# Kernel optimization log

Hardware: AMD Instinct MI355X
Metric: run time of the kernel (lower is better)

Reference implementation:

```python
import jax, jax.numpy as jnp
import numpy as np


def setup_inputs() -> dict:
    key = jax.random.key(0)
    ks = jax.random.split(key, 6)
    B, T, U = 4, 160, 80
    De, Dd = 640, 640
    inner, vocab = 640, 1024
    return {
        "enc_state": jax.random.normal(ks[0], (B, T, De), jnp.float32),
        "dec_state": jax.random.normal(ks[1], (B, U, Dd), jnp.float32),
        "W1": jax.random.normal(ks[2], (De + Dd, inner), jnp.float32) * (1.0 / np.sqrt(De + Dd)),
        "b1": jax.random.normal(ks[3], (inner,), jnp.float32) * 0.02,
        "W2": jax.random.normal(ks[4], (inner, vocab), jnp.float32) * (1.0 / np.sqrt(inner)),
        "b2": jax.random.normal(ks[5], (vocab,), jnp.float32) * 0.02,
    }


def reference(enc_state, dec_state, W1, b1, W2, b2):
    # Faithful to: cat([enc tiled over U, dec tiled over T], -1) @ W1 + b1,
    # algebraically split so the [B,T,U,2D] concat is never materialized:
    # cat(e, d) @ W1 == e @ W1[:De] + d @ W1[De:]
    De = enc_state.shape[-1]
    W1_enc, W1_dec = W1[:De], W1[De:]
    enc_proj = jnp.einsum("btd,dh->bth", enc_state, W1_enc)   # [B,T,H]
    dec_proj = jnp.einsum("bud,dh->buh", dec_state, W1_dec)   # [B,U,H]
    # broadcast add over the (T,U) lattice -> [B,T,U,H]
    hidden = jnp.tanh(enc_proj[:, :, None, :] + dec_proj[:, None, :, :] + b1)
    logits = jnp.einsum("btuh,hv->btuv", hidden, W2) + b2     # [B,T,U,V]
    return logits
```

## Files before the change

### kernel.cpp

```cpp
#include <hip/hip_runtime.h>
#include <hip/hip_bf16.h>
#include <cstdint>

#define D_    640
#define V_    1024
#define M_    51200

typedef __bf16 bf16x8 __attribute__((ext_vector_type(8)));
typedef float floatx4 __attribute__((ext_vector_type(4)));

__device__ __forceinline__ void g2l16(const void* g, void* l) {
    __builtin_amdgcn_global_load_lds((const __attribute__((address_space(1))) void*)g,
                                     (__attribute__((address_space(3))) void*)l,
                                     16, 0, 0);
}

__device__ __forceinline__ float fast_tanh(float x) {
    float e = __builtin_amdgcn_exp2f(x * 2.8853900817779268f);
    return 1.0f - 2.0f * __builtin_amdgcn_rcpf(e + 1.0f);
}

__global__ __launch_bounds__(256) void proj_kernel(
    const float* __restrict__ enc, const float* __restrict__ dec,
    const float* __restrict__ W1, const float* __restrict__ b1,
    float* __restrict__ encp, float* __restrict__ decp) {
    __shared__ float As[64][36];
    __shared__ float Ws[32][68];

    const int rt = blockIdx.y;
    const int ct = blockIdx.x;
    const bool is_enc = (rt < 10);
    const float* Asrc; const float* Wsrc; float* Cdst;
    if (is_enc) { Asrc = enc + (size_t)rt * 64 * D_;        Wsrc = W1;           Cdst = encp + (size_t)rt * 64 * D_; }
    else        { Asrc = dec + (size_t)(rt - 10) * 64 * D_; Wsrc = W1 + D_ * D_; Cdst = decp + (size_t)(rt - 10) * 64 * D_; }

    const int tid = threadIdx.x;
    const int ar = tid >> 2,  ac = (tid & 3) * 8;
    const int wr2 = tid >> 3, wc2 = (tid & 7) * 8;
    const int tr = tid >> 4,  tc = tid & 15;

    float acc[4][4] = {};
    for (int k0 = 0; k0 < D_; k0 += 32) {
        __syncthreads();
        *(floatx4*)&As[ar][ac]       = *(const floatx4*)&Asrc[(size_t)ar * D_ + k0 + ac];
        *(floatx4*)&As[ar][ac + 4]   = *(const floatx4*)&Asrc[(size_t)ar * D_ + k0 + ac + 4];
        *(floatx4*)&Ws[wr2][wc2]     = *(const floatx4*)&Wsrc[(size_t)(k0 + wr2) * D_ + ct * 64 + wc2];
        *(floatx4*)&Ws[wr2][wc2 + 4] = *(const floatx4*)&Wsrc[(size_t)(k0 + wr2) * D_ + ct * 64 + wc2 + 4];
        __syncthreads();
#pragma unroll
        for (int kk = 0; kk < 32; kk++) {
            floatx4 w = *(const floatx4*)&Ws[kk][tc * 4];
            float a0 = As[tr * 4 + 0][kk], a1 = As[tr * 4 + 1][kk];
            float a2 = As[tr * 4 + 2][kk], a3 = As[tr * 4 + 3][kk];
#pragma unroll
            for (int j = 0; j < 4; j++) {
                acc[0][j] += a0 * w[j]; acc[1][j] += a1 * w[j];
                acc[2][j] += a2 * w[j]; acc[3][j] += a3 * w[j];
            }
        }
    }
    floatx4 bv = {0.f, 0.f, 0.f, 0.f};
    if (is_enc) bv = *(const floatx4*)&b1[ct * 64 + tc * 4];
#pragma unroll
    for (int i = 0; i < 4; i++) {
        floatx4 v = { acc[i][0] + bv[0], acc[i][1] + bv[1],
                      acc[i][2] + bv[2], acc[i][3] + bv[3] };
        *(floatx4*)&Cdst[(size_t)(tr * 4 + i) * D_ + ct * 64 + tc * 4] = v;
    }
}

__global__ __launch_bounds__(256) void w2t_kernel(
    const float* __restrict__ W2, __bf16* __restrict__ W2t) {
    __shared__ __bf16 tile[32][33];
    const int vt = blockIdx.x;
    const int kt = blockIdx.y;
    const int tx = threadIdx.x & 31, ty = threadIdx.x >> 5;
#pragma unroll
    for (int i = 0; i < 4; i++)
        tile[ty + i * 8][tx] = (__bf16)W2[(size_t)(kt * 32 + ty + i * 8) * V_ + vt * 32 + tx];
    __syncthreads();
#pragma unroll
    for (int i = 0; i < 4; i++)
        W2t[(size_t)(vt * 32 + ty + i * 8) * D_ + kt * 32 + tx] = tile[tx][ty + i * 8];
}

__global__ __launch_bounds__(256, 2) void joint_kernel(
    const float* __restrict__ encp, const float* __restrict__ decp,
    const __bf16* __restrict__ W2t, const float* __restrict__ b2,
    float* __restrict__ C) {
    __shared__ __align__(128) char lds[81920];

    const int bid = blockIdx.x;
    const int swz = (bid & 7) * 200 + (bid >> 3);
    const int mt = swz >> 2, nt = swz & 3;
    const int m0 = mt * 128, n0 = nt * 256;

    const int tid = threadIdx.x;
    const int w = tid >> 6, l = tid & 63;
    const int lr = l & 15, lk = l >> 4;

    char* ldsp = (char*)lds;

    const char* Wb = (const char*)W2t
        + (size_t)(n0 + (tid >> 3)) * 1280
        + (unsigned)((((tid & 7) ^ ((tid >> 3) & 7)) * 16));
    const unsigned bdst = 16384u + (unsigned)tid * 16u;

    const int pr = tid >> 1;
    const int kh = (tid & 1) * 32;
    const int R  = m0 + pr;
    const int bt = R / 80;
    const int uu = R - bt * 80;
    const int drw = (bt / 160) * 80 + uu;
    const float* ep = encp + (size_t)bt * D_ + kh;
    const float* dp = decp + (size_t)drw * D_ + kh;
    const unsigned prb = (unsigned)(pr * 128);
    const unsigned ps0 = (unsigned)((tid & 1) * 4);
    const unsigned px  = (unsigned)(pr & 7);

    floatx4 acc[8][4] = {};

#define STAGE_B(BUF, T) do { \
    const char* _s = Wb + (size_t)(T) * 128; \
    char* _d = ldsp + bdst + (BUF) * 32768; \
    g2l16(_s,           _d); \
    g2l16(_s +  40960,  _d +  4096); \
    g2l16(_s +  81920,  _d +  8192); \
    g2l16(_s + 122880,  _d + 12288); \
    g2l16(_s + 163840,  _d + 16384); \
    g2l16(_s + 204800,  _d + 20480); \
    g2l16(_s + 245760,  _d + 24576); \
    g2l16(_s + 286720,  _d + 28672); \
  } while (0)

#define PRODUCE_A(T) do { \
    _Pragma("unroll") for (int sub = 0; sub < 2; ++sub) { \
      const float* _e = ep + (T) * 64 + sub * 16; \
      const float* _d = dp + (T) * 64 + sub * 16; \
      floatx4 ev[4], dv[4]; \
      _Pragma("unroll") for (int q = 0; q < 4; ++q) { \
        ev[q] = *(const floatx4*)(_e + q * 4); \
        dv[q] = *(const floatx4*)(_d + q * 4); \
      } \
      bf16x8 h0, h1; \
      _Pragma("unroll") for (int q = 0; q < 4; ++q) { \
        _Pragma("unroll") for (int i2 = 0; i2 < 4; ++i2) { \
          float t_ = fast_tanh(ev[q][i2] + dv[q][i2]); \
          if (q < 2) h0[q * 4 + i2] = (__bf16)t_; else h1[(q - 2) * 4 + i2] = (__bf16)t_; \
        } } \
      *(bf16x8*)(ldsp + prb + (((ps0 + sub * 2)     ^ px) * 16)) = h0; \
      *(bf16x8*)(ldsp + prb + (((ps0 + sub * 2 + 1) ^ px) * 16)) = h1; \
    } } while (0)

#define FRAGS_MFMA(BUF) do { \
    _Pragma("unroll") \
    for (int s = 0; s < 2; ++s) { \
        const unsigned sx = (unsigned)((((s * 4 + lk) ^ (lr & 7)) * 16)); \
        bf16x8 af[8], bfr[4]; \
        _Pragma("unroll") for (int i = 0; i < 8; ++i) \
            af[i] = *(const bf16x8*)(ldsp + (i * 16 + lr) * 128 + sx); \
        _Pragma("unroll") for (int j = 0; j < 4; ++j) \
            bfr[j] = *(const bf16x8*)(ldsp + 16384 + (BUF) * 32768 + (w * 64 + j * 16 + lr) * 128 + sx); \
        _Pragma("unroll") for (int i = 0; i < 8; ++i) \
            _Pragma("unroll") for (int j = 0; j < 4; ++j) \
                acc[i][j] = __builtin_amdgcn_mfma_f32_16x16x32_bf16(af[i], bfr[j], acc[i][j], 0, 0, 0); \
    } } while (0)

    STAGE_B(0, 0);
    PRODUCE_A(0);
    __syncthreads();

#pragma unroll 1
    for (int t = 0; t < 9; ++t) {
        const int buf = t & 1, nb = buf ^ 1;
        FRAGS_MFMA(buf);
        __syncthreads();
        STAGE_B(nb, t + 1);
        PRODUCE_A(t + 1);
        __syncthreads();
    }
    FRAGS_MFMA(1);

#pragma unroll
    for (int j = 0; j < 4; ++j) {
        const int col = n0 + w * 64 + j * 16 + lr;
        const float bj = b2[col];
#pragma unroll
        for (int i = 0; i < 8; ++i) {
            const int row = m0 + i * 16 + lk * 4;
            float* Cp = C + (size_t)row * V_ + col;
#pragma unroll
            for (int rg = 0; rg < 4; ++rg)
                Cp[(size_t)rg * V_] = acc[i][j][rg] + bj;
        }
    }
#undef STAGE_B
#undef PRODUCE_A
#undef FRAGS_MFMA
}

extern "C" void kernel_launch(void* const* d_in, const int* in_sizes, int n_in,
                              void* d_out, int out_size, void* d_ws, size_t ws_size,
                              hipStream_t stream) {
    const float* enc = (const float*)d_in[0];
    const float* dec = (const float*)d_in[1];
    const float* W1  = (const float*)d_in[2];
    const float* b1  = (const float*)d_in[3];
    const float* W2  = (const float*)d_in[4];
    const float* b2  = (const float*)d_in[5];
    float* out = (float*)d_out;

    char* ws = (char*)d_ws;
    float*  encp = (float*)ws;
    float*  decp = (float*)(ws + 1638400);
    __bf16* W2t  = (__bf16*)(ws + 1638400 + 819200);

    proj_kernel<<<dim3(10, 15), 256, 0, stream>>>(enc, dec, W1, b1, encp, decp);
    w2t_kernel<<<dim3(32, 20), 256, 0, stream>>>(W2, W2t);
    joint_kernel<<<1600, 256, 0, stream>>>(encp, decp, W2t, b2, out);
}
```

Measured before the change: 369.3 us.

## Load W2 fragments directly to registers, halve M tile, transpose MFMA for vector stores

The joint kernel stops staging W2t through LDS with global_load_lds. Each wave now loads its B fragments straight from global memory into double-buffered registers. The M tile is halved to 64 rows, so the grid doubles to 3200 blocks and LDS shrinks to 16 KB, which should raise occupancy. MFMA operands are swapped so each lane holds four consecutive columns, which allows float4 output stores and a float4 bias load. The trade-off is redundant W2 global reads per block, since each 256-column B tile now serves only 64 rows, plus reliance on L2 for B reuse and hand-placed barriers.

```diff
diff --git a/kernel.cpp b/kernel.cpp
--- a/kernel.cpp
+++ b/kernel.cpp
@@ -8,12 +8,6 @@
 
 typedef __bf16 bf16x8 __attribute__((ext_vector_type(8)));
 typedef float floatx4 __attribute__((ext_vector_type(4)));
-
-__device__ __forceinline__ void g2l16(const void* g, void* l) {
-    __builtin_amdgcn_global_load_lds((const __attribute__((address_space(1))) void*)g,
-                                     (__attribute__((address_space(3))) void*)l,
-                                     16, 0, 0);
-}
 
 __device__ __forceinline__ float fast_tanh(float x) {
     float e = __builtin_amdgcn_exp2f(x * 2.8853900817779268f);
@@ -88,12 +82,12 @@
     const float* __restrict__ encp, const float* __restrict__ decp,
     const __bf16* __restrict__ W2t, const float* __restrict__ b2,
     float* __restrict__ C) {
-    __shared__ __align__(128) char lds[81920];
+    __shared__ __align__(128) char lds[16384];
 
     const int bid = blockIdx.x;
-    const int swz = (bid & 7) * 200 + (bid >> 3);
+    const int swz = (bid & 7) * 400 + (bid >> 3);
     const int mt = swz >> 2, nt = swz & 3;
-    const int m0 = mt * 128, n0 = nt * 256;
+    const int m0 = mt * 64, n0 = nt * 256;
 
     const int tid = threadIdx.x;
     const int w = tid >> 6, l = tid & 63;
@@ -102,101 +96,97 @@
     char* ldsp = (char*)lds;
 
     const char* Wb = (const char*)W2t
-        + (size_t)(n0 + (tid >> 3)) * 1280
-        + (unsigned)((((tid & 7) ^ ((tid >> 3) & 7)) * 16));
-    const unsigned bdst = 16384u + (unsigned)tid * 16u;
-
-    const int pr = tid >> 1;
-    const int kh = (tid & 1) * 32;
+        + (size_t)(n0 + w * 64 + lr) * 1280 + (unsigned)(lk * 16);
+
+    const int pr = tid >> 2;
+    const int kq = tid & 3;
     const int R  = m0 + pr;
     const int bt = R / 80;
     const int uu = R - bt * 80;
     const int drw = (bt / 160) * 80 + uu;
-    const float* ep = encp + (size_t)bt * D_ + kh;
-    const float* dp = decp + (size_t)drw * D_ + kh;
+    const float* ep = encp + (size_t)bt * D_ + kq * 16;
+    const float* dp = decp + (size_t)drw * D_ + kq * 16;
     const unsigned prb = (unsigned)(pr * 128);
-    const unsigned ps0 = (unsigned)((tid & 1) * 4);
-    const unsigned px  = (unsigned)(pr & 7);
-
-    floatx4 acc[8][4] = {};
-
-#define STAGE_B(BUF, T) do { \
-    const char* _s = Wb + (size_t)(T) * 128; \
-    char* _d = ldsp + bdst + (BUF) * 32768; \
-    g2l16(_s,           _d); \
-    g2l16(_s +  40960,  _d +  4096); \
-    g2l16(_s +  81920,  _d +  8192); \
-    g2l16(_s + 122880,  _d + 12288); \
-    g2l16(_s + 163840,  _d + 16384); \
-    g2l16(_s + 204800,  _d + 20480); \
-    g2l16(_s + 245760,  _d + 24576); \
-    g2l16(_s + 286720,  _d + 28672); \
+    const unsigned pw0 = prb + (unsigned)((((kq * 2)     ^ (pr & 7)) * 16));
+    const unsigned pw1 = prb + (unsigned)((((kq * 2 + 1) ^ (pr & 7)) * 16));
+
+    floatx4 accT[4][4] = {};
+
+#define LOAD_BFR(DST, T) do { \
+    const char* _b = Wb + (size_t)(T) * 128; \
+    _Pragma("unroll") for (int j = 0; j < 4; ++j) { \
+        DST[j]     = *(const bf16x8*)(_b + (size_t)(j * 16) * 1280); \
+        DST[j + 4] = *(const bf16x8*)(_b + (size_t)(j * 16) * 1280 + 64); \
+    } } while (0)
+
+#define PRODUCE_A(BUF, T) do { \
+    const float* _e = ep + (T) * 64; const float* _d = dp + (T) * 64; \
+    floatx4 ev[4], dv[4]; \
+    _Pragma("unroll") for (int q = 0; q < 4; ++q) { \
+      ev[q] = *(const floatx4*)(_e + q * 4); \
+      dv[q] = *(const floatx4*)(_d + q * 4); \
+    } \
+    bf16x8 h0, h1; \
+    _Pragma("unroll") for (int q = 0; q < 4; ++q) \
+      _Pragma("unroll") for (int i2 = 0; i2 < 4; ++i2) { \
+        float t_ = fast_tanh(ev[q][i2] + dv[q][i2]); \
+        if (q < 2) h0[q * 4 + i2] = (__bf16)t_; else h1[(q - 2) * 4 + i2] = (__bf16)t_; \
+      } \
+    *(bf16x8*)(ldsp + (BUF) * 8192 + pw0) = h0; \
+    *(bf16x8*)(ldsp + (BUF) * 8192 + pw1) = h1; \
   } while (0)
 
-#define PRODUCE_A(T) do { \
-    _Pragma("unroll") for (int sub = 0; sub < 2; ++sub) { \
-      const float* _e = ep + (T) * 64 + sub * 16; \
-      const float* _d = dp + (T) * 64 + sub * 16; \
-      floatx4 ev[4], dv[4]; \
-      _Pragma("unroll") for (int q = 0; q < 4; ++q) { \
-        ev[q] = *(const floatx4*)(_e + q * 4); \
-        dv[q] = *(const floatx4*)(_d + q * 4); \
-      } \
-      bf16x8 h0, h1; \
-      _Pragma("unroll") for (int q = 0; q < 4; ++q) { \
-        _Pragma("unroll") for (int i2 = 0; i2 < 4; ++i2) { \
-          float t_ = fast_tanh(ev[q][i2] + dv[q][i2]); \
-          if (q < 2) h0[q * 4 + i2] = (__bf16)t_; else h1[(q - 2) * 4 + i2] = (__bf16)t_; \
-        } } \
-      *(bf16x8*)(ldsp + prb + (((ps0 + sub * 2)     ^ px) * 16)) = h0; \
-      *(bf16x8*)(ldsp + prb + (((ps0 + sub * 2 + 1) ^ px) * 16)) = h1; \
+#define FRAGS_MFMA(BUF, BFR) do { \
+    _Pragma("unroll") for (int s = 0; s < 2; ++s) { \
+        const unsigned sx = (unsigned)((((s * 4 + lk) ^ (lr & 7)) * 16)); \
+        bf16x8 af[4]; \
+        _Pragma("unroll") for (int i = 0; i < 4; ++i) \
+            af[i] = *(const bf16x8*)(ldsp + (BUF) * 8192 + (i * 16 + lr) * 128 + sx); \
+        _Pragma("unroll") for (int j = 0; j < 4; ++j) \
+            _Pragma("unroll") for (int i = 0; i < 4; ++i) \
+                accT[j][i] = __builtin_amdgcn_mfma_f32_16x16x32_bf16(BFR[s * 4 + j], af[i], accT[j][i], 0, 0, 0); \
     } } while (0)
 
-#define FRAGS_MFMA(BUF) do { \
-    _Pragma("unroll") \
-    for (int s = 0; s < 2; ++s) { \
-        const unsigned sx = (unsigned)((((s * 4 + lk) ^ (lr & 7)) * 16)); \
-        bf16x8 af[8], bfr[4]; \
-        _Pragma("unroll") for (int i = 0; i < 8; ++i) \
-            af[i] = *(const bf16x8*)(ldsp + (i * 16 + lr) * 128 + sx); \
-        _Pragma("unroll") for (int j = 0; j < 4; ++j) \
-            bfr[j] = *(const bf16x8*)(ldsp + 16384 + (BUF) * 32768 + (w * 64 + j * 16 + lr) * 128 + sx); \
-        _Pragma("unroll") for (int i = 0; i < 8; ++i) \
-            _Pragma("unroll") for (int j = 0; j < 4; ++j) \
-                acc[i][j] = __builtin_amdgcn_mfma_f32_16x16x32_bf16(af[i], bfr[j], acc[i][j], 0, 0, 0); \
-    } } while (0)
-
-    STAGE_B(0, 0);
-    PRODUCE_A(0);
-    __syncthreads();
+#define ABAR do { \
+    asm volatile("s_waitcnt lgkmcnt(0)" ::: "memory"); \
+    __builtin_amdgcn_s_barrier(); \
+    __builtin_amdgcn_sched_barrier(0); \
+  } while (0)
+
+    bf16x8 bA[8], bB[8];
+
+    LOAD_BFR(bA, 0);
+    PRODUCE_A(0, 0);
+    ABAR;
 
 #pragma unroll 1
-    for (int t = 0; t < 9; ++t) {
-        const int buf = t & 1, nb = buf ^ 1;
-        FRAGS_MFMA(buf);
-        __syncthreads();
-        STAGE_B(nb, t + 1);
-        PRODUCE_A(t + 1);
-        __syncthreads();
-    }
-    FRAGS_MFMA(1);
+    for (int t = 0; t < 10; t += 2) {
+        LOAD_BFR(bB, t + 1);
+        FRAGS_MFMA(0, bA);
+        PRODUCE_A(1, t + 1);
+        ABAR;
+        if (t < 8) LOAD_BFR(bA, t + 2);
+        FRAGS_MFMA(1, bB);
+        if (t < 8) PRODUCE_A(0, t + 2);
+        ABAR;
+    }
 
 #pragma unroll
     for (int j = 0; j < 4; ++j) {
-        const int col = n0 + w * 64 + j * 16 + lr;
-        const float bj = b2[col];
-#pragma unroll
-        for (int i = 0; i < 8; ++i) {
-            const int row = m0 + i * 16 + lk * 4;
-            float* Cp = C + (size_t)row * V_ + col;
-#pragma unroll
-            for (int rg = 0; rg < 4; ++rg)
-                Cp[(size_t)rg * V_] = acc[i][j][rg] + bj;
+        const int col0 = n0 + w * 64 + j * 16 + lk * 4;
+        const floatx4 bv = *(const floatx4*)&b2[col0];
+#pragma unroll
+        for (int i = 0; i < 4; ++i) {
+            const int row = m0 + i * 16 + lr;
+            floatx4 v = { accT[j][i][0] + bv[0], accT[j][i][1] + bv[1],
+                          accT[j][i][2] + bv[2], accT[j][i][3] + bv[3] };
+            *(floatx4*)&C[(size_t)row * V_ + col0] = v;
         }
     }
-#undef STAGE_B
+#undef LOAD_BFR
 #undef PRODUCE_A
 #undef FRAGS_MFMA
+#undef ABAR
 }
 
 extern "C" void kernel_launch(void* const* d_in, const int* in_sizes, int n_in,
@@ -217,5 +207,5 @@
 
     proj_kernel<<<dim3(10, 15), 256, 0, stream>>>(enc, dec, W1, b1, encp, decp);
     w2t_kernel<<<dim3(32, 20), 256, 0, stream>>>(W2, W2t);
-    joint_kernel<<<1600, 256, 0, stream>>>(encp, decp, W2t, b2, out);
-}
+    joint_kernel<<<3200, 256, 0, stream>>>(encp, decp, W2t, b2, out);
+}
```

After: 416.1 us. 12.7% more time.

## Split fused tanh-GEMM into separate hidden materialization and bf16 GEMM kernels

Applied to the files above, without the earlier changes.

Replaces the fused joint kernel, which computed tanh(enc+dec) inside the GEMM prologue, with a standalone kernel that writes the bf16 hidden tensor to workspace, followed by a pure bf16 GEMM. The GEMM now stages both A and B through global_load_lds with a K-step of 32 and a smaller LDS footprint, prefetching the next tile before the MFMAs. It also swaps the MFMA operands so the epilogue writes C with vectorized float4 stores instead of scalar ones. In exchange, a ~65MB hidden tensor is written and read back through memory, and an extra kernel launch is added.

```diff
diff --git a/kernel.cpp b/kernel.cpp
--- a/kernel.cpp
+++ b/kernel.cpp
@@ -84,11 +84,35 @@
         W2t[(size_t)(vt * 32 + ty + i * 8) * D_ + kt * 32 + tx] = tile[tx][ty + i * 8];
 }
 
-__global__ __launch_bounds__(256, 2) void joint_kernel(
+__global__ __launch_bounds__(256) void hidden_kernel(
     const float* __restrict__ encp, const float* __restrict__ decp,
-    const __bf16* __restrict__ W2t, const float* __restrict__ b2,
-    float* __restrict__ C) {
-    __shared__ __align__(128) char lds[81920];
+    __bf16* __restrict__ H) {
+    const unsigned g = blockIdx.x * 256u + threadIdx.x;
+    const unsigned row = g / 80u;
+    const unsigned hg  = g % 80u;
+    const unsigned u   = row % 80u;
+    const unsigned bt  = row / 80u;
+    const unsigned b   = bt / 160u;
+
+    const float* ep = encp + (size_t)bt * D_ + hg * 8;
+    const float* dp = decp + (size_t)(b * 80u + u) * D_ + hg * 8;
+
+    floatx4 e0 = *(const floatx4*)ep, e1 = *(const floatx4*)(ep + 4);
+    floatx4 d0 = *(const floatx4*)dp, d1 = *(const floatx4*)(dp + 4);
+
+    bf16x8 hv;
+#pragma unroll
+    for (int i = 0; i < 4; i++) hv[i]     = (__bf16)fast_tanh(e0[i] + d0[i]);
+#pragma unroll
+    for (int i = 0; i < 4; i++) hv[i + 4] = (__bf16)fast_tanh(e1[i] + d1[i]);
+
+    *(bf16x8*)(H + (size_t)g * 8) = hv;
+}
+
+__global__ __launch_bounds__(256, 2) void gemm_kernel(
+    const __bf16* __restrict__ H, const __bf16* __restrict__ W2t,
+    const float* __restrict__ b2, float* __restrict__ C) {
+    __shared__ __align__(128) char lds[49152];
 
     const int bid = blockIdx.x;
     const int swz = (bid & 7) * 200 + (bid >> 3);
@@ -101,101 +125,64 @@
 
     char* ldsp = (char*)lds;
 
-    const char* Wb = (const char*)W2t
-        + (size_t)(n0 + (tid >> 3)) * 1280
-        + (unsigned)((((tid & 7) ^ ((tid >> 3) & 7)) * 16));
-    const unsigned bdst = 16384u + (unsigned)tid * 16u;
-
-    const int pr = tid >> 1;
-    const int kh = (tid & 1) * 32;
-    const int R  = m0 + pr;
-    const int bt = R / 80;
-    const int uu = R - bt * 80;
-    const int drw = (bt / 160) * 80 + uu;
-    const float* ep = encp + (size_t)bt * D_ + kh;
-    const float* dp = decp + (size_t)drw * D_ + kh;
-    const unsigned prb = (unsigned)(pr * 128);
-    const unsigned ps0 = (unsigned)((tid & 1) * 4);
-    const unsigned px  = (unsigned)(pr & 7);
-
-    floatx4 acc[8][4] = {};
-
+    const int srow = tid >> 2;
+    const int sphy = tid & 3;
+    const unsigned scol = (unsigned)((sphy ^ ((srow >> 1) & 3)) * 16);
+    const char* Ag = (const char*)H   + (size_t)(m0 + srow) * 1280 + scol;
+    const char* Bg = (const char*)W2t + (size_t)(n0 + srow) * 1280 + scol;
+    const unsigned sdst = (unsigned)tid * 16u;
+
+    const unsigned px16 = (unsigned)((lk ^ ((lr >> 1) & 3)) * 16);
+
+    floatx4 accT[4][8] = {};
+
+#define STAGE_A(BUF, T) do { \
+    g2l16(Ag + (T) * 64,          ldsp + (BUF) * 8192 + sdst); \
+    g2l16(Ag + 81920 + (T) * 64,  ldsp + (BUF) * 8192 + sdst + 4096); \
+  } while (0)
 #define STAGE_B(BUF, T) do { \
-    const char* _s = Wb + (size_t)(T) * 128; \
-    char* _d = ldsp + bdst + (BUF) * 32768; \
-    g2l16(_s,           _d); \
-    g2l16(_s +  40960,  _d +  4096); \
-    g2l16(_s +  81920,  _d +  8192); \
-    g2l16(_s + 122880,  _d + 12288); \
-    g2l16(_s + 163840,  _d + 16384); \
-    g2l16(_s + 204800,  _d + 20480); \
-    g2l16(_s + 245760,  _d + 24576); \
-    g2l16(_s + 286720,  _d + 28672); \
+    g2l16(Bg + (T) * 64,           ldsp + 16384 + (BUF) * 16384 + sdst); \
+    g2l16(Bg +  81920 + (T) * 64,  ldsp + 16384 + (BUF) * 16384 + sdst + 4096); \
+    g2l16(Bg + 163840 + (T) * 64,  ldsp + 16384 + (BUF) * 16384 + sdst + 8192); \
+    g2l16(Bg + 245760 + (T) * 64,  ldsp + 16384 + (BUF) * 16384 + sdst + 12288); \
   } while (0)
 
-#define PRODUCE_A(T) do { \
-    _Pragma("unroll") for (int sub = 0; sub < 2; ++sub) { \
-      const float* _e = ep + (T) * 64 + sub * 16; \
-      const float* _d = dp + (T) * 64 + sub * 16; \
-      floatx4 ev[4], dv[4]; \
-      _Pragma("unroll") for (int q = 0; q < 4; ++q) { \
-        ev[q] = *(const floatx4*)(_e + q * 4); \
-        dv[q] = *(const floatx4*)(_d + q * 4); \
-      } \
-      bf16x8 h0, h1; \
-      _Pragma("unroll") for (int q = 0; q < 4; ++q) { \
-        _Pragma("unroll") for (int i2 = 0; i2 < 4; ++i2) { \
-          float t_ = fast_tanh(ev[q][i2] + dv[q][i2]); \
-          if (q < 2) h0[q * 4 + i2] = (__bf16)t_; else h1[(q - 2) * 4 + i2] = (__bf16)t_; \
-        } } \
-      *(bf16x8*)(ldsp + prb + (((ps0 + sub * 2)     ^ px) * 16)) = h0; \
-      *(bf16x8*)(ldsp + prb + (((ps0 + sub * 2 + 1) ^ px) * 16)) = h1; \
-    } } while (0)
-
 #define FRAGS_MFMA(BUF) do { \
-    _Pragma("unroll") \
-    for (int s = 0; s < 2; ++s) { \
-        const unsigned sx = (unsigned)((((s * 4 + lk) ^ (lr & 7)) * 16)); \
-        bf16x8 af[8], bfr[4]; \
+    bf16x8 af[8], bfr[4]; \
+    _Pragma("unroll") for (int i = 0; i < 8; ++i) \
+        af[i] = *(const bf16x8*)(ldsp + (BUF) * 8192 + (i * 16 + lr) * 64 + px16); \
+    _Pragma("unroll") for (int j = 0; j < 4; ++j) \
+        bfr[j] = *(const bf16x8*)(ldsp + 16384 + (BUF) * 16384 + (w * 64 + j * 16 + lr) * 64 + px16); \
+    _Pragma("unroll") for (int j = 0; j < 4; ++j) \
         _Pragma("unroll") for (int i = 0; i < 8; ++i) \
-            af[i] = *(const bf16x8*)(ldsp + (i * 16 + lr) * 128 + sx); \
-        _Pragma("unroll") for (int j = 0; j < 4; ++j) \
-            bfr[j] = *(const bf16x8*)(ldsp + 16384 + (BUF) * 32768 + (w * 64 + j * 16 + lr) * 128 + sx); \
-        _Pragma("unroll") for (int i = 0; i < 8; ++i) \
-            _Pragma("unroll") for (int j = 0; j < 4; ++j) \
-                acc[i][j] = __builtin_amdgcn_mfma_f32_16x16x32_bf16(af[i], bfr[j], acc[i][j], 0, 0, 0); \
-    } } while (0)
-
-    STAGE_B(0, 0);
-    PRODUCE_A(0);
+            accT[j][i] = __builtin_amdgcn_mfma_f32_16x16x32_bf16(bfr[j], af[i], accT[j][i], 0, 0, 0); \
+  } while (0)
+
+    STAGE_A(0, 0); STAGE_B(0, 0);
     __syncthreads();
 
 #pragma unroll 1
-    for (int t = 0; t < 9; ++t) {
+    for (int t = 0; t < 20; ++t) {
         const int buf = t & 1, nb = buf ^ 1;
+        if (t < 19) { STAGE_A(nb, t + 1); STAGE_B(nb, t + 1); }
         FRAGS_MFMA(buf);
         __syncthreads();
-        STAGE_B(nb, t + 1);
-        PRODUCE_A(t + 1);
-        __syncthreads();
-    }
-    FRAGS_MFMA(1);
+    }
 
 #pragma unroll
     for (int j = 0; j < 4; ++j) {
-        const int col = n0 + w * 64 + j * 16 + lr;
-        const float bj = b2[col];
+        const int col0 = n0 + w * 64 + j * 16 + lk * 4;
+        const floatx4 bv = *(const floatx4*)&b2[col0];
 #pragma unroll
         for (int i = 0; i < 8; ++i) {
-            const int row = m0 + i * 16 + lk * 4;
-            float* Cp = C + (size_t)row * V_ + col;
-#pragma unroll
-            for (int rg = 0; rg < 4; ++rg)
-                Cp[(size_t)rg * V_] = acc[i][j][rg] + bj;
+            const int row = m0 + i * 16 + lr;
+            floatx4 v = { accT[j][i][0] + bv[0], accT[j][i][1] + bv[1],
+                          accT[j][i][2] + bv[2], accT[j][i][3] + bv[3] };
+            *(floatx4*)&C[(size_t)row * V_ + col0] = v;
         }
     }
+#undef STAGE_A
 #undef STAGE_B
-#undef PRODUCE_A
 #undef FRAGS_MFMA
 }
 
@@ -214,8 +201,10 @@
     float*  encp = (float*)ws;
     float*  decp = (float*)(ws + 1638400);
     __bf16* W2t  = (__bf16*)(ws + 1638400 + 819200);
+    __bf16* Hbuf = (__bf16*)(ws + 1638400 + 819200 + 1310720);
 
     proj_kernel<<<dim3(10, 15), 256, 0, stream>>>(enc, dec, W1, b1, encp, decp);
     w2t_kernel<<<dim3(32, 20), 256, 0, stream>>>(W2, W2t);
-    joint_kernel<<<1600, 256, 0, stream>>>(encp, decp, W2t, b2, out);
-}
+    hidden_kernel<<<16000, 256, 0, stream>>>(encp, decp, Hbuf);
+    gemm_kernel<<<1600, 256, 0, stream>>>(Hbuf, W2t, b2, out);
+}
```

Result: faster. 355.9 us (-3.6%).
